# Kernel tuning notes

Hardware: AMD Instinct MI355X
Metric: run time of the kernel (lower is better)

## Reference

```python
import jax, jax.numpy as jnp
import numpy as np


def setup_inputs() -> dict:
    key = jax.random.key(0)
    ks = jax.random.split(key, 6)
    N, E, D = 50000, 500000, 128
    H, O = 256, 128
    x = jax.random.normal(ks[0], (N, D), dtype=jnp.float32)
    edge_attr = jax.random.normal(ks[1], (E, D), dtype=jnp.float32)
    edge_index = jax.random.randint(ks[2], (E, 2), 0, N, dtype=jnp.int64)
    # MLP params, scaled like torch default init
    W1 = jax.random.normal(ks[3], (3 * D, H), dtype=jnp.float32) / np.sqrt(3 * D)
    b1 = jnp.zeros((H,), dtype=jnp.float32)
    W2 = jax.random.normal(ks[4], (H, O), dtype=jnp.float32) / np.sqrt(H)
    b2 = jnp.zeros((O,), dtype=jnp.float32)
    return {"x": x, "edge_attr": edge_attr, "W1": W1, "b1": b1,
            "W2": W2, "b2": b2, "edge_index": edge_index}


def reference(x, edge_attr, W1, b1, W2, b2, edge_index):
    # edge_index: [E, 2]; column 0 = sender, column 1 = receiver
    sender = x[edge_index[:, 0]]    # [E, D] gather
    receiver = x[edge_index[:, 1]]  # [E, D] gather
    feat = jnp.concatenate([sender, receiver, edge_attr], axis=-1)  # [E, 3D]
    h = jax.nn.relu(feat @ W1 + b1)  # [E, H]
    return h @ W2 + b2               # [E, O]
```

## Files before the change

kernel.cpp:

```cpp
#include <hip/hip_runtime.h>
#include <hip/hip_bf16.h>

#define D 128
#define K1 384
#define H 256
#define O 128
#define BE 64
#define GRIDP 256
#define LDF (K1 + 8)
#define LDHF (H + 8)

typedef __attribute__((ext_vector_type(8))) short bf16x8;
typedef __attribute__((ext_vector_type(4))) float f32x4;

#define SSW(row, col) ((row) * 128 + ((col) ^ (((row) & 7) << 3)))
#define HSW(row, col) ((row) * 256 + ((col) ^ (((row) & 7) << 3)))

#define LGKM_BARRIER()                                                 \
    do {                                                               \
        asm volatile("s_waitcnt lgkmcnt(0)\n\ts_barrier" ::: "memory");\
        __builtin_amdgcn_sched_barrier(0);                             \
    } while (0)

__device__ inline ushort f2b(float f) {
    union { float f; unsigned u; } v; v.f = f;
    unsigned u = v.u;
    unsigned r = (u + 0x7fffu + ((u >> 16) & 1u)) >> 16;
    return (ushort)r;
}
__device__ inline ushort4 cvt4(float4 v) {
    ushort4 u; u.x = f2b(v.x); u.y = f2b(v.y); u.z = f2b(v.z); u.w = f2b(v.w); return u;
}
__device__ inline bf16x8 cvt8(f32x4 a, f32x4 b) {
    union { bf16x8 v; ushort u[8]; } w;
    w.u[0] = f2b(a[0]); w.u[1] = f2b(a[1]); w.u[2] = f2b(a[2]); w.u[3] = f2b(a[3]);
    w.u[4] = f2b(b[0]); w.u[5] = f2b(b[1]); w.u[6] = f2b(b[2]); w.u[7] = f2b(b[3]);
    return w.v;
}

__global__ void prep_weights(const float* __restrict__ W1, const float* __restrict__ W2,
                             ushort* __restrict__ W1t, ushort* __restrict__ W2t) {
    int tid = blockIdx.x * blockDim.x + threadIdx.x;
    if (tid < 256 * 384) {
        int n = tid / 384, k = tid % 384;
        W1t[tid] = f2b(W1[k * 256 + n]);
    } else {
        int t2 = tid - 256 * 384;
        if (t2 < 128 * 256) {
            int o = t2 / 256, k = t2 % 256;
            W2t[t2] = f2b(W2[k * 128 + o]);
        }
    }
}

__global__ __launch_bounds__(256)
void prep_x(const float* __restrict__ x, ushort* __restrict__ Xb, long total8) {
    long t = (long)blockIdx.x * blockDim.x + threadIdx.x;
    if (t < total8) {
        const float* src = x + t * 8;
        float4 v0 = ((const float4*)src)[0], v1 = ((const float4*)src)[1];
        union { bf16x8 v; ushort4 u[2]; } w;
        w.u[0] = cvt4(v0); w.u[1] = cvt4(v1);
        *(bf16x8*)(Xb + t * 8) = w.v;
    }
}

__global__ __launch_bounds__(512, 2)
void edge_mlp9(const float* __restrict__ ea, const int* __restrict__ eidx,
               const ushort* __restrict__ Xb,
               const ushort* __restrict__ W1t, const ushort* __restrict__ W2t,
               const float* __restrict__ b1, const float* __restrict__ b2,
               float* __restrict__ out, int E, int ntiles) {
    __shared__ __align__(16) ushort sBuf[24576];
    ushort* s0 = sBuf;
    ushort* s1 = sBuf + 8192;
    ushort* s2 = sBuf + 16384;
    ushort* sH = sBuf;

    const int tid = threadIdx.x;
    const int wave = tid >> 6, lane = tid & 63;
    const int row16 = lane & 15, kgrp = lane >> 4;
    const int srow = tid >> 3, oct = tid & 7;

    bf16x8 w1f[12][2];
    #pragma unroll
    for (int ks = 0; ks < 12; ++ks)
        #pragma unroll
        for (int fc = 0; fc < 2; ++fc)
            w1f[ks][fc] = *(const bf16x8*)(W1t + (wave * 32 + fc * 16 + row16) * K1 + ks * 32 + kgrp * 8);
    bf16x8 w2f[8];
    #pragma unroll
    for (int ks = 0; ks < 8; ++ks)
        w2f[ks] = *(const bf16x8*)(W2t + (wave * 16 + row16) * H + ks * 32 + kgrp * 8);
    const float b1v0 = b1[wave * 32 + row16];
    const float b1v1 = b1[wave * 32 + 16 + row16];
    const float b2v  = b2[wave * 16 + row16];

    int t = blockIdx.x;
    if (t >= ntiles) return;

    bf16x8 pxs[2], pxr[2];
    f32x4  pea[4];

    {
        long se = (long)t * BE + srow; if (se >= E) se = E - 1;
        int2 ei = *(const int2*)(eidx + 2 * se);
        const ushort* ps = Xb + (long)ei.x * D + oct * 16;
        const ushort* pr = Xb + (long)ei.y * D + oct * 16;
        const float*  pe = ea + se * D + oct * 16;
        #pragma unroll
        for (int j = 0; j < 2; ++j) pxs[j] = *(const bf16x8*)(ps + j * 8);
        #pragma unroll
        for (int j = 0; j < 2; ++j) pxr[j] = *(const bf16x8*)(pr + j * 8);
        #pragma unroll
        for (int j = 0; j < 4; ++j) pea[j] = ((const f32x4*)pe)[j];

        #pragma unroll
        for (int j = 0; j < 2; ++j) *(bf16x8*)(s0 + SSW(srow, oct * 16 + j * 8)) = pxs[j];
        #pragma unroll
        for (int j = 0; j < 2; ++j) *(bf16x8*)(s1 + SSW(srow, oct * 16 + j * 8)) = pxr[j];
        *(bf16x8*)(s2 + SSW(srow, oct * 16 + 0)) = cvt8(pea[0], pea[1]);
        *(bf16x8*)(s2 + SSW(srow, oct * 16 + 8)) = cvt8(pea[2], pea[3]);
    }

    int tn = t + GRIDP;
    int2 ei2;
    {
        int tc = (tn < ntiles) ? tn : (ntiles - 1);
        long se = (long)tc * BE + srow; if (se >= E) se = E - 1;
        ei2 = *(const int2*)(eidx + 2 * se);
    }

    while (true) {
        LGKM_BARRIER();
        const bool hasNext = (tn < ntiles);
        if (hasNext) {
            long sen = (long)tn * BE + srow; if (sen >= E) sen = E - 1;
            const ushort* ps = Xb + (long)ei2.x * D + oct * 16;
            const ushort* pr = Xb + (long)ei2.y * D + oct * 16;
            const float*  pe = ea + sen * D + oct * 16;
            #pragma unroll
            for (int j = 0; j < 2; ++j) pxs[j] = *(const bf16x8*)(ps + j * 8);
            #pragma unroll
            for (int j = 0; j < 2; ++j) pxr[j] = *(const bf16x8*)(pr + j * 8);
            #pragma unroll
            for (int j = 0; j < 4; ++j) pea[j] = ((const f32x4*)pe)[j];
            int tnn = tn + GRIDP;
            int tc = (tnn < ntiles) ? tnn : (ntiles - 1);
            long se2 = (long)tc * BE + srow; if (se2 >= E) se2 = E - 1;
            ei2 = *(const int2*)(eidx + 2 * se2);
        }

        f32x4 acc[4][2];
        #pragma unroll
        for (int fr = 0; fr < 4; ++fr) { acc[fr][0] = (f32x4){0,0,0,0}; acc[fr][1] = (f32x4){0,0,0,0}; }

        #pragma unroll
        for (int ks = 0; ks < 12; ++ks) {
            const ushort* sA = (ks < 4) ? s0 : ((ks < 8) ? s1 : s2);
            const int kl = (ks & 3) * 32 + kgrp * 8;
            bf16x8 a[4];
            #pragma unroll
            for (int fr = 0; fr < 4; ++fr)
                a[fr] = *(const bf16x8*)(sA + SSW(fr * 16 + row16, kl));
            #pragma unroll
            for (int fr = 0; fr < 4; ++fr) {
                acc[fr][0] = __builtin_amdgcn_mfma_f32_16x16x32_bf16(a[fr], w1f[ks][0], acc[fr][0], 0, 0, 0);
                acc[fr][1] = __builtin_amdgcn_mfma_f32_16x16x32_bf16(a[fr], w1f[ks][1], acc[fr][1], 0, 0, 0);
            }
        }
        LGKM_BARRIER();

        #pragma unroll
        for (int fr = 0; fr < 4; ++fr)
            #pragma unroll
            for (int r = 0; r < 4; ++r) {
                int row = fr * 16 + kgrp * 4 + r;
                int swz = (row & 7) << 3;
                sH[row * 256 + ((wave * 32 + row16) ^ swz)]      = f2b(fmaxf(acc[fr][0][r] + b1v0, 0.f));
                sH[row * 256 + ((wave * 32 + 16 + row16) ^ swz)] = f2b(fmaxf(acc[fr][1][r] + b1v1, 0.f));
            }
        LGKM_BARRIER();

        f32x4 acc2[4];
        #pragma unroll
        for (int fr = 0; fr < 4; ++fr) acc2[fr] = (f32x4){0,0,0,0};
        #pragma unroll
        for (int ks = 0; ks < 8; ++ks) {
            bf16x8 a[4];
            #pragma unroll
            for (int fr = 0; fr < 4; ++fr)
                a[fr] = *(const bf16x8*)(sH + HSW(fr * 16 + row16, ks * 32 + kgrp * 8));
            #pragma unroll
            for (int fr = 0; fr < 4; ++fr)
                acc2[fr] = __builtin_amdgcn_mfma_f32_16x16x32_bf16(a[fr], w2f[ks], acc2[fr], 0, 0, 0);
        }
        {
            const long e0 = (long)t * BE;
            #pragma unroll
            for (int fr = 0; fr < 4; ++fr)
                #pragma unroll
                for (int r = 0; r < 4; ++r) {
                    long erow = e0 + fr * 16 + kgrp * 4 + r;
                    if (erow < E) out[erow * O + wave * 16 + row16] = acc2[fr][r] + b2v;
                }
        }

        if (!hasNext) break;
        LGKM_BARRIER();
        #pragma unroll
        for (int j = 0; j < 2; ++j) *(bf16x8*)(s0 + SSW(srow, oct * 16 + j * 8)) = pxs[j];
        #pragma unroll
        for (int j = 0; j < 2; ++j) *(bf16x8*)(s1 + SSW(srow, oct * 16 + j * 8)) = pxr[j];
        *(bf16x8*)(s2 + SSW(srow, oct * 16 + 0)) = cvt8(pea[0], pea[1]);
        *(bf16x8*)(s2 + SSW(srow, oct * 16 + 8)) = cvt8(pea[2], pea[3]);

        t = tn; tn += GRIDP;
    }
}

__global__ __launch_bounds__(256, 2)
void edge_mlp(const float* __restrict__ x, const float* __restrict__ ea,
              const int* __restrict__ eidx,
              const float* __restrict__ b1, const float* __restrict__ b2,
              const ushort* __restrict__ W1t, const ushort* __restrict__ W2t,
              float* __restrict__ out, int E) {
    __shared__ ushort sF[64 * LDF];
    ushort* sH = sF;
    const int tid = threadIdx.x, wave = tid >> 6, lane = tid & 63;
    const int row16 = lane & 15, kgrp = lane >> 4;
    const long e0 = (long)blockIdx.x * 64;
    {
        int i = tid >> 2, p = tid & 3;
        long e = e0 + i; if (e >= E) e = E - 1;
        int s = eidx[2 * e], r = eidx[2 * e + 1];
        const float* src0 = x + (long)s * D + p * 32;
        const float* src1 = x + (long)r * D + p * 32;
        const float* src2 = ea + e * D + p * 32;
        ushort* dst = sF + i * LDF + p * 32;
        #pragma unroll
        for (int j = 0; j < 8; ++j) *(ushort4*)(dst + 0 * D + j * 4) = cvt4(((const float4*)src0)[j]);
        #pragma unroll
        for (int j = 0; j < 8; ++j) *(ushort4*)(dst + 1 * D + j * 4) = cvt4(((const float4*)src1)[j]);
        #pragma unroll
        for (int j = 0; j < 8; ++j) *(ushort4*)(dst + 2 * D + j * 4) = cvt4(((const float4*)src2)[j]);
    }
    __syncthreads();
    f32x4 acc[4][4];
    #pragma unroll
    for (int a = 0; a < 4; ++a)
        #pragma unroll
        for (int b = 0; b < 4; ++b) acc[a][b] = (f32x4){0,0,0,0};
    const int wcol = wave * 64;
    for (int k0 = 0; k0 < K1; k0 += 32) {
        bf16x8 a[4], b[4];
        #pragma unroll
        for (int fr = 0; fr < 4; ++fr)
            a[fr] = *(const bf16x8*)(sF + (fr * 16 + row16) * LDF + k0 + kgrp * 8);
        #pragma unroll
        for (int fc = 0; fc < 4; ++fc)
            b[fc] = *(const bf16x8*)(W1t + (wcol + fc * 16 + row16) * K1 + k0 + kgrp * 8);
        #pragma unroll
        for (int fr = 0; fr < 4; ++fr)
            #pragma unroll
            for (int fc = 0; fc < 4; ++fc)
                acc[fr][fc] = __builtin_amdgcn_mfma_f32_16x16x32_bf16(a[fr], b[fc], acc[fr][fc], 0, 0, 0);
    }
    __syncthreads();
    #pragma unroll
    for (int fc = 0; fc < 4; ++fc) {
        int col = wcol + fc * 16 + row16;
        float bv = b1[col];
        #pragma unroll
        for (int fr = 0; fr < 4; ++fr)
            #pragma unroll
            for (int r = 0; r < 4; ++r) {
                int row = fr * 16 + kgrp * 4 + r;
                sH[row * LDHF + col] = f2b(fmaxf(acc[fr][fc][r] + bv, 0.f));
            }
    }
    __syncthreads();
    f32x4 acc2[4][2];
    #pragma unroll
    for (int a = 0; a < 4; ++a)
        #pragma unroll
        for (int b = 0; b < 2; ++b) acc2[a][b] = (f32x4){0,0,0,0};
    const int wo = wave * 32;
    for (int k0 = 0; k0 < H; k0 += 32) {
        bf16x8 a[4], b[2];
        #pragma unroll
        for (int fr = 0; fr < 4; ++fr)
            a[fr] = *(const bf16x8*)(sH + (fr * 16 + row16) * LDHF + k0 + kgrp * 8);
        #pragma unroll
        for (int fc = 0; fc < 2; ++fc)
            b[fc] = *(const bf16x8*)(W2t + (wo + fc * 16 + row16) * H + k0 + kgrp * 8);
        #pragma unroll
        for (int fr = 0; fr < 4; ++fr)
            #pragma unroll
            for (int fc = 0; fc < 2; ++fc)
                acc2[fr][fc] = __builtin_amdgcn_mfma_f32_16x16x32_bf16(a[fr], b[fc], acc2[fr][fc], 0, 0, 0);
    }
    #pragma unroll
    for (int fc = 0; fc < 2; ++fc) {
        int col = wo + fc * 16 + row16;
        float bv = b2[col];
        #pragma unroll
        for (int fr = 0; fr < 4; ++fr)
            #pragma unroll
            for (int r = 0; r < 4; ++r) {
                long row = e0 + fr * 16 + kgrp * 4 + r;
                if (row < E) out[row * O + col] = acc2[fr][fc][r] + bv;
            }
    }
}

extern "C" void kernel_launch(void* const* d_in, const int* in_sizes, int n_in,
                              void* d_out, int out_size, void* d_ws, size_t ws_size,
                              hipStream_t stream) {
    const float* x  = (const float*)d_in[0];
    const float* ea = (const float*)d_in[1];
    const float* W1 = (const float*)d_in[2];
    const float* b1 = (const float*)d_in[3];
    const float* W2 = (const float*)d_in[4];
    const float* b2 = (const float*)d_in[5];
    const int* eidx = (const int*)d_in[6];
    float* out = (float*)d_out;

    const int E = in_sizes[1] / D;
    const int N = in_sizes[0] / D;

    ushort* W1t = (ushort*)d_ws;
    ushort* W2t = W1t + 256 * 384;
    ushort* Xb  = W2t + 128 * 256;
    size_t need = ((size_t)(256 * 384 + 128 * 256) + (size_t)N * 128) * 2;

    prep_weights<<<512, 256, 0, stream>>>(W1, W2, W1t, W2t);

    if (ws_size >= need) {
        long total8 = (long)N * D / 8;
        int nbx = (int)((total8 + 255) / 256);
        prep_x<<<nbx, 256, 0, stream>>>(x, Xb, total8);
        int ntiles = (E + BE - 1) / BE;
        int grid = (ntiles < GRIDP) ? ntiles : GRIDP;
        edge_mlp9<<<grid, 512, 0, stream>>>(ea, eidx, Xb, W1t, W2t, b1, b2, out, E, ntiles);
    } else {
        int nb = (E + 63) / 64;
        edge_mlp<<<nb, 256, 0, stream>>>(x, ea, eidx, b1, b2, W1t, W2t, out, E);
    }
}
```

Baseline: 216.4 us.

## Use 4 waves per block with wider per-wave output tiles in edge MLP

The persistent edge-MLP kernel drops from 8 waves of 512 threads to 4 waves of 256 threads. Each wave now computes 64 hidden columns and 32 output columns, holding twice as many register-resident weight fragments, and each thread gathers twice as much data per row. The aim is more MFMA work per LDS A-fragment load, fewer waves contending for LDS, and less barrier overhead. In exchange, register pressure roughly doubles (about 192 VGPRs for W1 alone), latency hiding drops, and the grid still fixes 256 blocks, so the device carries only half as many waves in flight.

```diff
diff --git a/kernel.cpp b/kernel.cpp
--- a/kernel.cpp
+++ b/kernel.cpp
@@ -65,12 +65,12 @@
     }
 }
 
-__global__ __launch_bounds__(512, 2)
-void edge_mlp9(const float* __restrict__ ea, const int* __restrict__ eidx,
-               const ushort* __restrict__ Xb,
-               const ushort* __restrict__ W1t, const ushort* __restrict__ W2t,
-               const float* __restrict__ b1, const float* __restrict__ b2,
-               float* __restrict__ out, int E, int ntiles) {
+__global__ __launch_bounds__(256, 1)
+void edge_mlp10(const float* __restrict__ ea, const int* __restrict__ eidx,
+                const ushort* __restrict__ Xb,
+                const ushort* __restrict__ W1t, const ushort* __restrict__ W2t,
+                const float* __restrict__ b1, const float* __restrict__ b2,
+                float* __restrict__ out, int E, int ntiles) {
     __shared__ __align__(16) ushort sBuf[24576];
     ushort* s0 = sBuf;
     ushort* s1 = sBuf + 8192;
@@ -80,47 +80,53 @@
     const int tid = threadIdx.x;
     const int wave = tid >> 6, lane = tid & 63;
     const int row16 = lane & 15, kgrp = lane >> 4;
-    const int srow = tid >> 3, oct = tid & 7;
-
-    bf16x8 w1f[12][2];
+    const int srow = tid >> 2, sq = tid & 3;
+
+    bf16x8 w1f[12][4];
     #pragma unroll
     for (int ks = 0; ks < 12; ++ks)
         #pragma unroll
+        for (int fc = 0; fc < 4; ++fc)
+            w1f[ks][fc] = *(const bf16x8*)(W1t + (wave * 64 + fc * 16 + row16) * K1 + ks * 32 + kgrp * 8);
+    bf16x8 w2f[8][2];
+    #pragma unroll
+    for (int ks = 0; ks < 8; ++ks)
+        #pragma unroll
         for (int fc = 0; fc < 2; ++fc)
-            w1f[ks][fc] = *(const bf16x8*)(W1t + (wave * 32 + fc * 16 + row16) * K1 + ks * 32 + kgrp * 8);
-    bf16x8 w2f[8];
-    #pragma unroll
-    for (int ks = 0; ks < 8; ++ks)
-        w2f[ks] = *(const bf16x8*)(W2t + (wave * 16 + row16) * H + ks * 32 + kgrp * 8);
-    const float b1v0 = b1[wave * 32 + row16];
-    const float b1v1 = b1[wave * 32 + 16 + row16];
-    const float b2v  = b2[wave * 16 + row16];
+            w2f[ks][fc] = *(const bf16x8*)(W2t + (wave * 32 + fc * 16 + row16) * H + ks * 32 + kgrp * 8);
+    float b1v[4];
+    #pragma unroll
+    for (int fc = 0; fc < 4; ++fc) b1v[fc] = b1[wave * 64 + fc * 16 + row16];
+    float b2v[2];
+    #pragma unroll
+    for (int fc = 0; fc < 2; ++fc) b2v[fc] = b2[wave * 32 + fc * 16 + row16];
 
     int t = blockIdx.x;
     if (t >= ntiles) return;
 
-    bf16x8 pxs[2], pxr[2];
-    f32x4  pea[4];
+    bf16x8 pxs[4], pxr[4];
+    f32x4  pea[8];
 
     {
         long se = (long)t * BE + srow; if (se >= E) se = E - 1;
         int2 ei = *(const int2*)(eidx + 2 * se);
-        const ushort* ps = Xb + (long)ei.x * D + oct * 16;
-        const ushort* pr = Xb + (long)ei.y * D + oct * 16;
-        const float*  pe = ea + se * D + oct * 16;
-        #pragma unroll
-        for (int j = 0; j < 2; ++j) pxs[j] = *(const bf16x8*)(ps + j * 8);
-        #pragma unroll
-        for (int j = 0; j < 2; ++j) pxr[j] = *(const bf16x8*)(pr + j * 8);
-        #pragma unroll
-        for (int j = 0; j < 4; ++j) pea[j] = ((const f32x4*)pe)[j];
-
-        #pragma unroll
-        for (int j = 0; j < 2; ++j) *(bf16x8*)(s0 + SSW(srow, oct * 16 + j * 8)) = pxs[j];
-        #pragma unroll
-        for (int j = 0; j < 2; ++j) *(bf16x8*)(s1 + SSW(srow, oct * 16 + j * 8)) = pxr[j];
-        *(bf16x8*)(s2 + SSW(srow, oct * 16 + 0)) = cvt8(pea[0], pea[1]);
-        *(bf16x8*)(s2 + SSW(srow, oct * 16 + 8)) = cvt8(pea[2], pea[3]);
+        const ushort* ps = Xb + (long)ei.x * D + sq * 32;
+        const ushort* pr = Xb + (long)ei.y * D + sq * 32;
+        const float*  pe = ea + se * D + sq * 32;
+        #pragma unroll
+        for (int j = 0; j < 4; ++j) pxs[j] = *(const bf16x8*)(ps + j * 8);
+        #pragma unroll
+        for (int j = 0; j < 4; ++j) pxr[j] = *(const bf16x8*)(pr + j * 8);
+        #pragma unroll
+        for (int j = 0; j < 8; ++j) pea[j] = ((const f32x4*)pe)[j];
+
+        #pragma unroll
+        for (int j = 0; j < 4; ++j) *(bf16x8*)(s0 + SSW(srow, sq * 32 + j * 8)) = pxs[j];
+        #pragma unroll
+        for (int j = 0; j < 4; ++j) *(bf16x8*)(s1 + SSW(srow, sq * 32 + j * 8)) = pxr[j];
+        #pragma unroll
+        for (int j = 0; j < 4; ++j)
+            *(bf16x8*)(s2 + SSW(srow, sq * 32 + j * 8)) = cvt8(pea[2 * j], pea[2 * j + 1]);
     }
 
     int tn = t + GRIDP;
@@ -136,24 +142,26 @@
         const bool hasNext = (tn < ntiles);
         if (hasNext) {
             long sen = (long)tn * BE + srow; if (sen >= E) sen = E - 1;
-            const ushort* ps = Xb + (long)ei2.x * D + oct * 16;
-            const ushort* pr = Xb + (long)ei2.y * D + oct * 16;
-            const float*  pe = ea + sen * D + oct * 16;
-            #pragma unroll
-            for (int j = 0; j < 2; ++j) pxs[j] = *(const bf16x8*)(ps + j * 8);
-            #pragma unroll
-            for (int j = 0; j < 2; ++j) pxr[j] = *(const bf16x8*)(pr + j * 8);
-            #pragma unroll
-            for (int j = 0; j < 4; ++j) pea[j] = ((const f32x4*)pe)[j];
+            const ushort* ps = Xb + (long)ei2.x * D + sq * 32;
+            const ushort* pr = Xb + (long)ei2.y * D + sq * 32;
+            const float*  pe = ea + sen * D + sq * 32;
+            #pragma unroll
+            for (int j = 0; j < 4; ++j) pxs[j] = *(const bf16x8*)(ps + j * 8);
+            #pragma unroll
+            for (int j = 0; j < 4; ++j) pxr[j] = *(const bf16x8*)(pr + j * 8);
+            #pragma unroll
+            for (int j = 0; j < 8; ++j) pea[j] = ((const f32x4*)pe)[j];
             int tnn = tn + GRIDP;
             int tc = (tnn < ntiles) ? tnn : (ntiles - 1);
             long se2 = (long)tc * BE + srow; if (se2 >= E) se2 = E - 1;
             ei2 = *(const int2*)(eidx + 2 * se2);
         }
 
-        f32x4 acc[4][2];
-        #pragma unroll
-        for (int fr = 0; fr < 4; ++fr) { acc[fr][0] = (f32x4){0,0,0,0}; acc[fr][1] = (f32x4){0,0,0,0}; }
+        f32x4 acc[4][4];
+        #pragma unroll
+        for (int fr = 0; fr < 4; ++fr)
+            #pragma unroll
+            for (int fc = 0; fc < 4; ++fc) acc[fr][fc] = (f32x4){0,0,0,0};
 
         #pragma unroll
         for (int ks = 0; ks < 12; ++ks) {
@@ -164,10 +172,10 @@
             for (int fr = 0; fr < 4; ++fr)
                 a[fr] = *(const bf16x8*)(sA + SSW(fr * 16 + row16, kl));
             #pragma unroll
-            for (int fr = 0; fr < 4; ++fr) {
-                acc[fr][0] = __builtin_amdgcn_mfma_f32_16x16x32_bf16(a[fr], w1f[ks][0], acc[fr][0], 0, 0, 0);
-                acc[fr][1] = __builtin_amdgcn_mfma_f32_16x16x32_bf16(a[fr], w1f[ks][1], acc[fr][1], 0, 0, 0);
-            }
+            for (int fr = 0; fr < 4; ++fr)
+                #pragma unroll
+                for (int fc = 0; fc < 4; ++fc)
+                    acc[fr][fc] = __builtin_amdgcn_mfma_f32_16x16x32_bf16(a[fr], w1f[ks][fc], acc[fr][fc], 0, 0, 0);
         }
         LGKM_BARRIER();
 
@@ -177,14 +185,16 @@
             for (int r = 0; r < 4; ++r) {
                 int row = fr * 16 + kgrp * 4 + r;
                 int swz = (row & 7) << 3;
-                sH[row * 256 + ((wave * 32 + row16) ^ swz)]      = f2b(fmaxf(acc[fr][0][r] + b1v0, 0.f));
-                sH[row * 256 + ((wave * 32 + 16 + row16) ^ swz)] = f2b(fmaxf(acc[fr][1][r] + b1v1, 0.f));
+                #pragma unroll
+                for (int fc = 0; fc < 4; ++fc)
+                    sH[row * 256 + ((wave * 64 + fc * 16 + row16) ^ swz)] =
+                        f2b(fmaxf(acc[fr][fc][r] + b1v[fc], 0.f));
             }
         LGKM_BARRIER();
 
-        f32x4 acc2[4];
-        #pragma unroll
-        for (int fr = 0; fr < 4; ++fr) acc2[fr] = (f32x4){0,0,0,0};
+        f32x4 acc2[4][2];
+        #pragma unroll
+        for (int fr = 0; fr < 4; ++fr) { acc2[fr][0] = (f32x4){0,0,0,0}; acc2[fr][1] = (f32x4){0,0,0,0}; }
         #pragma unroll
         for (int ks = 0; ks < 8; ++ks) {
             bf16x8 a[4];
@@ -192,28 +202,33 @@
             for (int fr = 0; fr < 4; ++fr)
                 a[fr] = *(const bf16x8*)(sH + HSW(fr * 16 + row16, ks * 32 + kgrp * 8));
             #pragma unroll
-            for (int fr = 0; fr < 4; ++fr)
-                acc2[fr] = __builtin_amdgcn_mfma_f32_16x16x32_bf16(a[fr], w2f[ks], acc2[fr], 0, 0, 0);
+            for (int fr = 0; fr < 4; ++fr) {
+                acc2[fr][0] = __builtin_amdgcn_mfma_f32_16x16x32_bf16(a[fr], w2f[ks][0], acc2[fr][0], 0, 0, 0);
+                acc2[fr][1] = __builtin_amdgcn_mfma_f32_16x16x32_bf16(a[fr], w2f[ks][1], acc2[fr][1], 0, 0, 0);
+            }
         }
         {
             const long e0 = (long)t * BE;
             #pragma unroll
-            for (int fr = 0; fr < 4; ++fr)
+            for (int fc = 0; fc < 2; ++fc)
                 #pragma unroll
-                for (int r = 0; r < 4; ++r) {
-                    long erow = e0 + fr * 16 + kgrp * 4 + r;
-                    if (erow < E) out[erow * O + wave * 16 + row16] = acc2[fr][r] + b2v;
-                }
+                for (int fr = 0; fr < 4; ++fr)
+                    #pragma unroll
+                    for (int r = 0; r < 4; ++r) {
+                        long erow = e0 + fr * 16 + kgrp * 4 + r;
+                        if (erow < E) out[erow * O + wave * 32 + fc * 16 + row16] = acc2[fr][fc][r] + b2v[fc];
+                    }
         }
 
         if (!hasNext) break;
         LGKM_BARRIER();
         #pragma unroll
-        for (int j = 0; j < 2; ++j) *(bf16x8*)(s0 + SSW(srow, oct * 16 + j * 8)) = pxs[j];
-        #pragma unroll
-        for (int j = 0; j < 2; ++j) *(bf16x8*)(s1 + SSW(srow, oct * 16 + j * 8)) = pxr[j];
-        *(bf16x8*)(s2 + SSW(srow, oct * 16 + 0)) = cvt8(pea[0], pea[1]);
-        *(bf16x8*)(s2 + SSW(srow, oct * 16 + 8)) = cvt8(pea[2], pea[3]);
+        for (int j = 0; j < 4; ++j) *(bf16x8*)(s0 + SSW(srow, sq * 32 + j * 8)) = pxs[j];
+        #pragma unroll
+        for (int j = 0; j < 4; ++j) *(bf16x8*)(s1 + SSW(srow, sq * 32 + j * 8)) = pxr[j];
+        #pragma unroll
+        for (int j = 0; j < 4; ++j)
+            *(bf16x8*)(s2 + SSW(srow, sq * 32 + j * 8)) = cvt8(pea[2 * j], pea[2 * j + 1]);
 
         t = tn; tn += GRIDP;
     }
@@ -342,7 +357,7 @@
         prep_x<<<nbx, 256, 0, stream>>>(x, Xb, total8);
         int ntiles = (E + BE - 1) / BE;
         int grid = (ntiles < GRIDP) ? ntiles : GRIDP;
-        edge_mlp9<<<grid, 512, 0, stream>>>(ea, eidx, Xb, W1t, W2t, b1, b2, out, E, ntiles);
+        edge_mlp10<<<grid, 256, 0, stream>>>(ea, eidx, Xb, W1t, W2t, b1, b2, out, E, ntiles);
     } else {
         int nb = (E + 63) / 64;
         edge_mlp<<<nb, 256, 0, stream>>>(x, ea, eidx, b1, b2, W1t, W2t, out, E);
```

Measured after the change: 304.2 us. 40.6% more time.

## Double-buffer the edge feature tile in LDS and drop two barriers per tile

Applied to the files above, without the earlier changes.

Splits LDS into two 48 KB feature buffers plus a separate hidden-activation buffer. The next tile's gathered features are written into the alternate buffer while the current one is read, which removes the barrier after GEMM1 and the barrier before the next tile's LDS stores. LDS use grows from 48 KB to 128 KB per block, which may cut occupancy below the two blocks per CU that the launch bounds request.

```diff
diff --git a/kernel.cpp b/kernel.cpp
--- a/kernel.cpp
+++ b/kernel.cpp
@@ -66,16 +66,13 @@
 }
 
 __global__ __launch_bounds__(512, 2)
-void edge_mlp9(const float* __restrict__ ea, const int* __restrict__ eidx,
-               const ushort* __restrict__ Xb,
-               const ushort* __restrict__ W1t, const ushort* __restrict__ W2t,
-               const float* __restrict__ b1, const float* __restrict__ b2,
-               float* __restrict__ out, int E, int ntiles) {
-    __shared__ __align__(16) ushort sBuf[24576];
-    ushort* s0 = sBuf;
-    ushort* s1 = sBuf + 8192;
-    ushort* s2 = sBuf + 16384;
-    ushort* sH = sBuf;
+void edge_mlp12(const float* __restrict__ ea, const int* __restrict__ eidx,
+                const ushort* __restrict__ Xb,
+                const ushort* __restrict__ W1t, const ushort* __restrict__ W2t,
+                const float* __restrict__ b1, const float* __restrict__ b2,
+                float* __restrict__ out, int E, int ntiles) {
+    __shared__ __align__(16) ushort sBuf[65536];
+    ushort* sH = sBuf + 49152;
 
     const int tid = threadIdx.x;
     const int wave = tid >> 6, lane = tid & 63;
@@ -116,13 +113,14 @@
         for (int j = 0; j < 4; ++j) pea[j] = ((const f32x4*)pe)[j];
 
         #pragma unroll
-        for (int j = 0; j < 2; ++j) *(bf16x8*)(s0 + SSW(srow, oct * 16 + j * 8)) = pxs[j];
-        #pragma unroll
-        for (int j = 0; j < 2; ++j) *(bf16x8*)(s1 + SSW(srow, oct * 16 + j * 8)) = pxr[j];
-        *(bf16x8*)(s2 + SSW(srow, oct * 16 + 0)) = cvt8(pea[0], pea[1]);
-        *(bf16x8*)(s2 + SSW(srow, oct * 16 + 8)) = cvt8(pea[2], pea[3]);
-    }
-
+        for (int j = 0; j < 2; ++j) *(bf16x8*)(sBuf + SSW(srow, oct * 16 + j * 8)) = pxs[j];
+        #pragma unroll
+        for (int j = 0; j < 2; ++j) *(bf16x8*)(sBuf + 8192 + SSW(srow, oct * 16 + j * 8)) = pxr[j];
+        *(bf16x8*)(sBuf + 16384 + SSW(srow, oct * 16 + 0)) = cvt8(pea[0], pea[1]);
+        *(bf16x8*)(sBuf + 16384 + SSW(srow, oct * 16 + 8)) = cvt8(pea[2], pea[3]);
+    }
+
+    int p = 0;
     int tn = t + GRIDP;
     int2 ei2;
     {
@@ -151,25 +149,25 @@
             ei2 = *(const int2*)(eidx + 2 * se2);
         }
 
+        const ushort* sA = sBuf + (p ? 24576 : 0);
         f32x4 acc[4][2];
         #pragma unroll
         for (int fr = 0; fr < 4; ++fr) { acc[fr][0] = (f32x4){0,0,0,0}; acc[fr][1] = (f32x4){0,0,0,0}; }
 
         #pragma unroll
         for (int ks = 0; ks < 12; ++ks) {
-            const ushort* sA = (ks < 4) ? s0 : ((ks < 8) ? s1 : s2);
+            const ushort* sP = sA + ((ks < 4) ? 0 : ((ks < 8) ? 8192 : 16384));
             const int kl = (ks & 3) * 32 + kgrp * 8;
             bf16x8 a[4];
             #pragma unroll
             for (int fr = 0; fr < 4; ++fr)
-                a[fr] = *(const bf16x8*)(sA + SSW(fr * 16 + row16, kl));
+                a[fr] = *(const bf16x8*)(sP + SSW(fr * 16 + row16, kl));
             #pragma unroll
             for (int fr = 0; fr < 4; ++fr) {
                 acc[fr][0] = __builtin_amdgcn_mfma_f32_16x16x32_bf16(a[fr], w1f[ks][0], acc[fr][0], 0, 0, 0);
                 acc[fr][1] = __builtin_amdgcn_mfma_f32_16x16x32_bf16(a[fr], w1f[ks][1], acc[fr][1], 0, 0, 0);
             }
         }
-        LGKM_BARRIER();
 
         #pragma unroll
         for (int fr = 0; fr < 4; ++fr)
@@ -207,15 +205,17 @@
         }
 
         if (!hasNext) break;
-        LGKM_BARRIER();
-        #pragma unroll
-        for (int j = 0; j < 2; ++j) *(bf16x8*)(s0 + SSW(srow, oct * 16 + j * 8)) = pxs[j];
-        #pragma unroll
-        for (int j = 0; j < 2; ++j) *(bf16x8*)(s1 + SSW(srow, oct * 16 + j * 8)) = pxr[j];
-        *(bf16x8*)(s2 + SSW(srow, oct * 16 + 0)) = cvt8(pea[0], pea[1]);
-        *(bf16x8*)(s2 + SSW(srow, oct * 16 + 8)) = cvt8(pea[2], pea[3]);
-
-        t = tn; tn += GRIDP;
+        {
+            ushort* sB = sBuf + (p ? 0 : 24576);
+            #pragma unroll
+            for (int j = 0; j < 2; ++j) *(bf16x8*)(sB + SSW(srow, oct * 16 + j * 8)) = pxs[j];
+            #pragma unroll
+            for (int j = 0; j < 2; ++j) *(bf16x8*)(sB + 8192 + SSW(srow, oct * 16 + j * 8)) = pxr[j];
+            *(bf16x8*)(sB + 16384 + SSW(srow, oct * 16 + 0)) = cvt8(pea[0], pea[1]);
+            *(bf16x8*)(sB + 16384 + SSW(srow, oct * 16 + 8)) = cvt8(pea[2], pea[3]);
+        }
+
+        p ^= 1; t = tn; tn += GRIDP;
     }
 }
 
@@ -342,7 +342,7 @@
         prep_x<<<nbx, 256, 0, stream>>>(x, Xb, total8);
         int ntiles = (E + BE - 1) / BE;
         int grid = (ntiles < GRIDP) ? ntiles : GRIDP;
-        edge_mlp9<<<grid, 512, 0, stream>>>(ea, eidx, Xb, W1t, W2t, b1, b2, out, E, ntiles);
+        edge_mlp12<<<grid, 512, 0, stream>>>(ea, eidx, Xb, W1t, W2t, b1, b2, out, E, ntiles);
     } else {
         int nb = (E + 63) / 64;
         edge_mlp<<<nb, 256, 0, stream>>>(x, ea, eidx, b1, b2, W1t, W2t, out, E);
```

Measured after the change: 249.8 us. 15.4% more time.
